# Optimization experiments

Hardware: AMD Instinct MI355X
Metric: run time of the kernel (lower is better)

## Reference

```python
import jax, jax.numpy as jnp
import numpy as np

B, N, C = 4096, 20, 512
S_VIEWS = 8
N_VIEWS = 20


def setup_inputs() -> dict:
    key = jax.random.key(0)
    k1, k2, k3, k4 = jax.random.split(key, 4)
    F0 = jax.random.normal(k1, (B, N, C), dtype=jnp.float32)
    vertices0 = jax.random.normal(k2, (B, N, 3), dtype=jnp.float32)
    W1 = jax.random.normal(k3, (C, 256), dtype=jnp.float32) * 0.04
    b1 = jnp.zeros((256,), dtype=jnp.float32)
    W2 = jax.random.normal(k4, (256, 40), dtype=jnp.float32) * 0.06
    b2 = jnp.zeros((40,), dtype=jnp.float32)
    return {"F0": F0, "vertices0": vertices0, "W1": W1, "b1": b1, "W2": W2, "b2": b2, "k": 8}


def _cls(x, W1, b1, W2, b2):
    # Linear(512,256) -> LeakyReLU(0.2) -> Linear(256,40)
    h = x @ W1 + b1
    h = jnp.where(h > 0, h, 0.2 * h)
    return h @ W2 + b2


def reference(F0, vertices0, W1, b1, W2, b2, k):
    # F0: [B, N, C]; vertices0: [B, N, 3]
    pooled_F = jnp.sum(F0, axis=1) / N_VIEWS                 # [B, C]
    pred = jnp.argmax(_cls(pooled_F, W1, b1, W2, b2), -1)    # [B] predicted class per sample
    score = _cls(F0, W1, b1, W2, b2)                         # [B, N, 40]
    # score[arange(B), :, pred] -> per-view score of the predicted class
    score_F = jnp.take_along_axis(score, pred[:, None, None], axis=2)[..., 0]  # [B, N]
    _, idx = jax.lax.top_k(score_F, S_VIEWS)                 # [B, S]
    F_new = jnp.take_along_axis(F0, idx[:, :, None], axis=1)            # [B, S, C]
    vertices_new = jnp.take_along_axis(vertices0, idx[:, :, None], axis=1)  # [B, S, 3]
    return (F_new, score, vertices_new)
```

## Files before the change

### kernel.cpp

```cpp
#include <hip/hip_runtime.h>
#include <cstdint>

#define BB 4096
#define NV 20
#define CC 512
#define HH 256
#define NC 40
#define SV 8
#define GG 3
#define TAU 2e-4f

typedef short short8 __attribute__((ext_vector_type(8)));
typedef float f32x4 __attribute__((ext_vector_type(4)));
typedef unsigned short ushort4v __attribute__((ext_vector_type(4)));

__device__ __forceinline__ unsigned short f2bf(float x) {
    unsigned u = __float_as_uint(x);
    unsigned r = (u + 0x7FFFu + ((u >> 16) & 1u)) >> 16;
    return (unsigned short)r;
}
__device__ __forceinline__ float bf2f(unsigned short h) {
    return __uint_as_float(((unsigned)h) << 16);
}

#define MFMA16(A, B, C) __builtin_amdgcn_mfma_f32_16x16x32_bf16(A, B, C, 0, 0, 0)
#define BC8(x) __builtin_bit_cast(short8, x)

__global__ void w1pack_kernel(const float* __restrict__ W1,
                              unsigned short* __restrict__ w1fh,
                              unsigned short* __restrict__ w1fl) {
    int e = blockIdx.x * 256 + threadIdx.x;
    int j3 = e & 7, kq = (e >> 3) & 3, n = (e >> 5) & 255, ks = e >> 13;
    int k = ks * 32 + kq * 8 + j3;
    float x = W1[k * HH + n];
    unsigned short h = f2bf(x);
    w1fh[e] = h;
    w1fl[e] = f2bf(x - bf2f(h));
}

__global__ void w2pack_kernel(const float* __restrict__ W2,
                              unsigned short* __restrict__ w2fh,
                              unsigned short* __restrict__ w2fl) {
    int e = blockIdx.x * 256 + threadIdx.x;
    int j3 = e & 7, kq = (e >> 3) & 3;
    int t = e >> 5;
    int n = t % 48, ks = t / 48;
    int k = ks * 32 + kq * 8 + j3;
    float x = (n < NC) ? W2[k * NC + n] : 0.f;
    unsigned short h = f2bf(x);
    w2fh[e] = h;
    w2fl[e] = f2bf(x - bf2f(h));
}

__global__ __launch_bounds__(256, 3) void fused_kernel(
    const float* __restrict__ F0, const float* __restrict__ V0,
    const float* __restrict__ W1, const float* __restrict__ b1,
    const float* __restrict__ W2, const float* __restrict__ b2,
    const unsigned short* __restrict__ w1fh, const unsigned short* __restrict__ w1fl,
    const unsigned short* __restrict__ w2fh, const unsigned short* __restrict__ w2fl,
    int* __restrict__ rflag, int* __restrict__ rpred,
    float* __restrict__ outF, float* __restrict__ outS, float* __restrict__ outV)
{
    const int blk = blockIdx.x;
    const int j = threadIdx.x;
    const int L = j & 63, wq = j >> 6, l15 = L & 15, kq = L >> 4;

    __shared__ __align__(16) char lds[46944];
    __shared__ int idx8[GG][SV];

    unsigned short* Ahi0 = (unsigned short*)lds;
    unsigned short* Alo0 = Ahi0 + 64 * 72;
    unsigned short* Ahi1 = (unsigned short*)(lds + 18432);
    unsigned short* Alo1 = Ahi1 + 64 * 72;
    unsigned short* Hhi  = (unsigned short*)lds;
    unsigned short* Hlo  = Hhi + 32 * 264;
    float*  Sc      = (float*)(lds + 36864);

    f32x4 acc[4][4];
#pragma unroll
    for (int mt = 0; mt < 4; ++mt)
#pragma unroll
        for (int nt = 0; nt < 4; ++nt) acc[mt][nt] = (f32x4){0.f, 0.f, 0.f, 0.f};

    const float4* srcp[4];
    int ldst[4];
    bool sval[4];
#pragma unroll
    for (int i = 0; i < 4; ++i) {
        int f = j + 256 * i;
        int row = f >> 4, k4 = f & 15;
        sval[i] = (row < 60);
        int bi = (row >= 40) ? 2 : (row >= 20) ? 1 : 0;
        int r = row - 20 * bi;
        int batch = blk * GG + bi; if (batch > BB - 1) batch = BB - 1;
        srcp[i] = (const float4*)(F0 + ((size_t)batch * NV + r) * CC) + k4;
        ldst[i] = row * 72 + k4 * 4;
    }

    float4 rv[4];
    auto STAGE_LOAD = [&](int kc) {
#pragma unroll
        for (int i = 0; i < 4; ++i)
            if (sval[i]) rv[i] = srcp[i][kc * 16];
    };
    auto STAGE_CONVERT = [&](unsigned short* __restrict__ Ah,
                             unsigned short* __restrict__ Al) {
#pragma unroll
        for (int i = 0; i < 4; ++i) {
            ushort4v hv = {0, 0, 0, 0}, lv = {0, 0, 0, 0};
            if (sval[i]) {
                float4 x = rv[i];
                hv.x = f2bf(x.x); lv.x = f2bf(x.x - bf2f(hv.x));
                hv.y = f2bf(x.y); lv.y = f2bf(x.y - bf2f(hv.y));
                hv.z = f2bf(x.z); lv.z = f2bf(x.z - bf2f(hv.z));
                hv.w = f2bf(x.w); lv.w = f2bf(x.w - bf2f(hv.w));
            }
            *(ushort4v*)&Ah[ldst[i]] = hv;
            *(ushort4v*)&Al[ldst[i]] = lv;
        }
    };

    const uint4* Bh = (const uint4*)w1fh;
    const uint4* Bl = (const uint4*)w1fl;

    STAGE_LOAD(0);
    STAGE_CONVERT(Ahi0, Alo0);
    STAGE_LOAD(1);
    __syncthreads();

    unsigned short *Ahc = Ahi0, *Alc = Alo0, *Ahn = Ahi1, *Aln = Alo1;
    for (int kc = 0; kc < 8; ++kc) {
        if (kc < 7) {
            STAGE_CONVERT(Ahn, Aln);
            if (kc < 6) STAGE_LOAD(kc + 2);
        }
#pragma unroll
        for (int ks_l = 0; ks_l < 2; ++ks_l) {
            int ks = kc * 2 + ks_l;
            uint4 bh[4], bl[4];
#pragma unroll
            for (int nt = 0; nt < 4; ++nt) {
                int bi1 = (ks * 256 + wq * 64 + nt * 16 + l15) * 4 + kq;
                bh[nt] = Bh[bi1]; bl[nt] = Bl[bi1];
            }
#pragma unroll
            for (int mt = 0; mt < 4; ++mt) {
                int off = (mt * 16 + l15) * 72 + ks_l * 32 + kq * 8;
                short8 Ah = BC8(*(const uint4*)&Ahc[off]);
                short8 Al = BC8(*(const uint4*)&Alc[off]);
#pragma unroll
                for (int nt = 0; nt < 4; ++nt) {
                    short8 Bhv = BC8(bh[nt]), Blv = BC8(bl[nt]);
                    acc[mt][nt] = MFMA16(Ah, Bhv, acc[mt][nt]);
                    acc[mt][nt] = MFMA16(Ah, Blv, acc[mt][nt]);
                    acc[mt][nt] = MFMA16(Al, Bhv, acc[mt][nt]);
                }
            }
        }
        __syncthreads();
        unsigned short* t;
        t = Ahc; Ahc = Ahn; Ahn = t;
        t = Alc; Alc = Aln; Aln = t;
    }

    const uint4* B2h = (const uint4*)w2fh;
    const uint4* B2l = (const uint4*)w2fl;
#pragma unroll
    for (int p = 0; p < 2; ++p) {
        __syncthreads();
#pragma unroll
        for (int mt2 = 0; mt2 < 2; ++mt2) {
            int mt = 2 * p + mt2;
            bool skip = (p == 1 && mt2 == 1 && kq == 3);
#pragma unroll
            for (int nt = 0; nt < 4; ++nt) {
                int col = wq * 64 + nt * 16 + l15;
                float bc = b1[col];
#pragma unroll
                for (int reg = 0; reg < 4; ++reg) {
                    int hb = mt2 * 16 + kq * 4 + reg;
                    float h = acc[mt][nt][reg] + bc;
                    h = (h > 0.f) ? h : 0.2f * h;
                    if (!skip) {
                        unsigned short hh = f2bf(h);
                        Hhi[hb * 264 + col] = hh;
                        Hlo[hb * 264 + col] = f2bf(h - bf2f(hh));
                    }
                }
            }
        }
        if (p == 1) {
#pragma unroll
            for (int nt = 0; nt < 4; ++nt) {
                int col = wq * 64 + nt * 16 + l15;
                float p0 = 0.f, p1 = 0.f, p2 = 0.f;
#pragma unroll
                for (int mt = 0; mt < 4; ++mt)
#pragma unroll
                    for (int reg = 0; reg < 4; ++reg) {
                        int g = mt * 16 + kq * 4 + reg;
                        float v = acc[mt][nt][reg];
                        p0 += (g < 20) ? v : 0.f;
                        p1 += (g >= 20 && g < 40) ? v : 0.f;
                        p2 += (g >= 40 && g < 60) ? v : 0.f;
                    }
                p0 += __shfl_xor(p0, 16); p0 += __shfl_xor(p0, 32);
                p1 += __shfl_xor(p1, 16); p1 += __shfl_xor(p1, 32);
                p2 += __shfl_xor(p2, 16); p2 += __shfl_xor(p2, 32);
                if (kq < 3) {
                    float s = (kq == 0) ? p0 : (kq == 1) ? p1 : p2;
                    float h = s * (1.0f / NV) + b1[col];
                    h = (h > 0.f) ? h : 0.2f * h;
                    unsigned short hh = f2bf(h);
                    Hhi[(28 + kq) * 264 + col] = hh;
                    Hlo[(28 + kq) * 264 + col] = f2bf(h - bf2f(hh));
                } else {
                    Hhi[31 * 264 + col] = 0;
                    Hlo[31 * 264 + col] = 0;
                }
            }
        }
        __syncthreads();

        if (wq < 3) {
            f32x4 sacc[2];
            sacc[0] = (f32x4){0.f, 0.f, 0.f, 0.f};
            sacc[1] = (f32x4){0.f, 0.f, 0.f, 0.f};
            for (int ks2 = 0; ks2 < 8; ++ks2) {
                int bi2 = (ks2 * 48 + wq * 16 + l15) * 4 + kq;
                short8 Bhv = BC8(B2h[bi2]), Blv = BC8(B2l[bi2]);
#pragma unroll
                for (int tt = 0; tt < 2; ++tt) {
                    int off = (tt * 16 + l15) * 264 + ks2 * 32 + kq * 8;
                    short8 Ah2 = BC8(*(const uint4*)&Hhi[off]);
                    short8 Al2 = BC8(*(const uint4*)&Hlo[off]);
                    sacc[tt] = MFMA16(Ah2, Bhv, sacc[tt]);
                    sacc[tt] = MFMA16(Ah2, Blv, sacc[tt]);
                    sacc[tt] = MFMA16(Al2, Bhv, sacc[tt]);
                }
            }
            int cls = wq * 16 + l15;
            if (cls < NC) {
                float bc2 = b2[cls];
#pragma unroll
                for (int tt = 0; tt < 2; ++tt)
#pragma unroll
                    for (int reg = 0; reg < 4; ++reg) {
                        int lm = 32 * p + tt * 16 + kq * 4 + reg;
                        float sv = sacc[tt][reg] + bc2;
                        if (lm < 60) {
                            int bi = (lm >= 40) ? 2 : (lm >= 20) ? 1 : 0;
                            int r = lm - 20 * bi;
                            Sc[bi * 840 + r * NC + cls] = sv;
                        } else if (lm < 63) {
                            Sc[(lm - 60) * 840 + NV * NC + cls] = sv;
                        }
                    }
            }
        }
    }
    __syncthreads();

    if (j < GG) {
        const float* sp = &Sc[j * 840 + NV * NC];
        int p = 0;
        float m1 = sp[0];
        for (int c = 1; c < NC; ++c)
            if (sp[c] > m1) { m1 = sp[c]; p = c; }
        float m2 = -1e30f;
        for (int c = 0; c < NC; ++c)
            if (c != p && sp[c] > m2) m2 = sp[c];
        int f0 = (m1 - m2 < TAU) ? 1 : 0;

        float v[NV];
#pragma unroll
        for (int n = 0; n < NV; ++n) v[n] = Sc[j * 840 + n * NC + p];
        int ord[9];
        float vals[9];
        unsigned taken = 0;
#pragma unroll
        for (int s = 0; s < 9; ++s) {
            int bi = 0;
            float bv = -1e30f;
#pragma unroll
            for (int n = 0; n < NV; ++n)
                if (!((taken >> n) & 1u) && v[n] > bv) { bv = v[n]; bi = n; }
            taken |= 1u << bi;
            ord[s] = bi;
            vals[s] = bv;
        }
        int fix = 0;
#pragma unroll
        for (int s = 0; s < 8; ++s)
            if (vals[s] - vals[s + 1] < TAU) fix = 1;
#pragma unroll
        for (int s = 0; s < SV; ++s) idx8[j][s] = ord[s];

        int batch = blk * GG + j; if (batch > BB - 1) batch = BB - 1;
        rflag[batch] = f0 ? 1 : (fix ? 2 : 0);
        rpred[batch] = p;
    }
    __syncthreads();

    for (int t = j; t < GG * NV * NC; t += 256) {
        int bi = t / 800, o = t - bi * 800;
        int batch = blk * GG + bi; if (batch > BB - 1) batch = BB - 1;
        outS[(size_t)batch * (NV * NC) + o] = Sc[bi * 840 + o];
    }

    for (int t = j; t < GG * SV * (CC / 4); t += 256) {
        int bi = t >> 10;
        int s = (t >> 7) & 7;
        int t4 = t & 127;
        int batch = blk * GG + bi; if (batch > BB - 1) batch = BB - 1;
        int row = idx8[bi][s];
        const float4* src = (const float4*)(F0 + ((size_t)batch * NV + row) * CC);
        float4* dst = (float4*)(outF + ((size_t)batch * SV + s) * CC);
        dst[t4] = src[t4];
    }

    if (j < GG * SV * 3) {
        int bi = j / 24, o = j - bi * 24;
        int s = o / 3, d = o - s * 3;
        int batch = blk * GG + bi; if (batch > BB - 1) batch = BB - 1;
        outV[((size_t)batch * SV + s) * 3 + d] =
            V0[((size_t)batch * NV + idx8[bi][s]) * 3 + d];
    }
}

__global__ __launch_bounds__(256) void rescue_kernel(
    const float* __restrict__ F0, const float* __restrict__ V0,
    const float* __restrict__ W1, const float* __restrict__ b1,
    const float* __restrict__ W2, const float* __restrict__ b2,
    const int* __restrict__ rflag, const int* __restrict__ rpred,
    float* __restrict__ outF, float* __restrict__ outV)
{
    const int b = blockIdx.x;
    const int flag = rflag[b];
    if (flag == 0) return;

    const int j = threadIdx.x;
    const int L = j & 63, wq = j >> 6;

    __shared__ __align__(16) float Xf[NV * CC];
    __shared__ double pooledD[CC];
    __shared__ double Dbuf[HH];
    __shared__ double Sd[NC];
    __shared__ double part[NV][4];
    __shared__ double SFdS[NV];
    __shared__ int predSh;
    __shared__ int idxs[SV];

    const float* Xb = F0 + (size_t)b * (NV * CC);
    for (int t = j; t < NV * CC / 4; t += 256)
        ((float4*)Xf)[t] = ((const float4*)Xb)[t];
    __syncthreads();

    if (flag == 1) {
        for (int c = j; c < CC; c += 256) {
            double s = 0.0;
            for (int r = 0; r < NV; ++r) s += (double)Xf[r * CC + c];
            pooledD[c] = s / (double)NV;
        }
        __syncthreads();
        double a = 0.0;
        for (int c = 0; c < CC; ++c) a += pooledD[c] * (double)W1[c * HH + j];
        double h = a + (double)b1[j];
        h = (h > 0.0) ? h : 0.2 * h;
        Dbuf[j] = h;
        __syncthreads();
        if (j < NC) {
            double s = 0.0;
            for (int k = 0; k < HH; ++k) s += Dbuf[k] * (double)W2[k * NC + j];
            Sd[j] = s + (double)b2[j];
        }
        __syncthreads();
        if (j == 0) {
            int p = 0;
            double m = Sd[0];
            for (int c = 1; c < NC; ++c)
                if (Sd[c] > m) { m = Sd[c]; p = c; }
            predSh = p;
        }
        __syncthreads();
    } else {
        if (j == 0) predSh = rpred[b];
        __syncthreads();
    }
    const int p = predSh;

    const double b1d = (double)b1[j];
    const double w2jp = (double)W2[j * NC + p];
#pragma unroll
    for (int half = 0; half < 2; ++half) {
        double a[10];
#pragma unroll
        for (int r = 0; r < 10; ++r) a[r] = 0.0;
        for (int c = 0; c < CC; c += 4) {
            double w0 = (double)W1[(c + 0) * HH + j];
            double w1v = (double)W1[(c + 1) * HH + j];
            double w2v = (double)W1[(c + 2) * HH + j];
            double w3v = (double)W1[(c + 3) * HH + j];
#pragma unroll
            for (int r = 0; r < 10; ++r) {
                const float4 x = *(const float4*)&Xf[(half * 10 + r) * CC + c];
                a[r] += (double)x.x * w0;
                a[r] += (double)x.y * w1v;
                a[r] += (double)x.z * w2v;
                a[r] += (double)x.w * w3v;
            }
        }
#pragma unroll
        for (int r = 0; r < 10; ++r) {
            double h = a[r] + b1d;
            h = (h > 0.0) ? h : 0.2 * h;
            double val = h * w2jp;
#pragma unroll
            for (int off = 32; off >= 1; off >>= 1)
                val += __shfl_xor(val, off);
            if (L == 0) part[half * 10 + r][wq] = val;
        }
    }
    __syncthreads();
    if (j < NV)
        SFdS[j] = part[j][0] + part[j][1] + part[j][2] + part[j][3]
                + (double)b2[p];
    __syncthreads();
    if (j == 0) {
        unsigned taken = 0;
        for (int s = 0; s < SV; ++s) {
            int bsel = 0;
            double bv = -1e300;
            for (int n = 0; n < NV; ++n)
                if (!((taken >> n) & 1u) && SFdS[n] > bv) { bv = SFdS[n]; bsel = n; }
            taken |= 1u << bsel;
            idxs[s] = bsel;
        }
    }
    __syncthreads();

    for (int t = j; t < SV * (CC / 4); t += 256) {
        int s = t >> 7, t4 = t & 127;
        int row = idxs[s];
        ((float4*)(outF + ((size_t)b * SV + s) * CC))[t4] =
            ((const float4*)(F0 + ((size_t)b * NV + row) * CC))[t4];
    }
    if (j < SV * 3) {
        int s = j / 3, d = j - s * 3;
        outV[((size_t)b * SV + s) * 3 + d] =
            V0[((size_t)b * NV + idxs[s]) * 3 + d];
    }
}

extern "C" void kernel_launch(void* const* d_in, const int* in_sizes, int n_in,
                              void* d_out, int out_size, void* d_ws, size_t ws_size,
                              hipStream_t stream) {
    const float* F0 = (const float*)d_in[0];
    const float* V0 = (const float*)d_in[1];
    const float* W1 = (const float*)d_in[2];
    const float* b1 = (const float*)d_in[3];
    const float* W2 = (const float*)d_in[4];
    const float* b2 = (const float*)d_in[5];

    char* ws = (char*)d_ws;
    unsigned short* w1fh = (unsigned short*)ws;
    unsigned short* w1fl = (unsigned short*)(ws + 262144);
    unsigned short* w2fh = (unsigned short*)(ws + 524288);
    unsigned short* w2fl = (unsigned short*)(ws + 548864);
    int* rflag = (int*)(ws + 573440);
    int* rpred = (int*)(ws + 589824);

    float* out = (float*)d_out;
    float* outF = out;
    float* outS = out + (size_t)BB * SV * CC;
    float* outV = outS + (size_t)BB * NV * NC;

    w1pack_kernel<<<512, 256, 0, stream>>>(W1, w1fh, w1fl);
    w2pack_kernel<<<48, 256, 0, stream>>>(W2, w2fh, w2fl);
    fused_kernel<<<(BB + GG - 1) / GG, 256, 0, stream>>>(
        F0, V0, W1, b1, W2, b2, w1fh, w1fl, w2fh, w2fl, rflag, rpred,
        outF, outS, outV);
    rescue_kernel<<<BB, 256, 0, stream>>>(
        F0, V0, W1, b1, W2, b2, rflag, rpred, outF, outV);
}
```

Measured before the change: 464.8 us.

## Compact rescue work into atomic worklist, fuse pack kernels, write scores directly

Merges the two weight-pack kernels into one launch that also resets a worklist counter. The fused kernel now writes per-view scores straight to global memory instead of staging them in LDS, which shrinks shared memory and raises the occupancy hint from 3 to 4 blocks. Flagged batches are appended to a compact worklist with an atomic, so the rescue kernel launches 256 persistent blocks that loop over it rather than 4096 mostly-empty blocks. The top-k selection now reads scores back from global memory, and the rescue kernel keeps 20 double accumulators per thread, which may raise register pressure.

Measured after the change: 693.6 us. +49.2%, slower.

```diff
diff --git a/kernel.cpp b/kernel.cpp
--- a/kernel.cpp
+++ b/kernel.cpp
@@ -26,46 +26,48 @@
 #define MFMA16(A, B, C) __builtin_amdgcn_mfma_f32_16x16x32_bf16(A, B, C, 0, 0, 0)
 #define BC8(x) __builtin_bit_cast(short8, x)
 
-__global__ void w1pack_kernel(const float* __restrict__ W1,
-                              unsigned short* __restrict__ w1fh,
-                              unsigned short* __restrict__ w1fl) {
+__global__ void pack_kernel(const float* __restrict__ W1,
+                            const float* __restrict__ W2,
+                            unsigned short* __restrict__ w1fh,
+                            unsigned short* __restrict__ w1fl,
+                            unsigned short* __restrict__ w2fh,
+                            unsigned short* __restrict__ w2fl,
+                            int* __restrict__ wcount) {
     int e = blockIdx.x * 256 + threadIdx.x;
-    int j3 = e & 7, kq = (e >> 3) & 3, n = (e >> 5) & 255, ks = e >> 13;
-    int k = ks * 32 + kq * 8 + j3;
-    float x = W1[k * HH + n];
-    unsigned short h = f2bf(x);
-    w1fh[e] = h;
-    w1fl[e] = f2bf(x - bf2f(h));
-}
-
-__global__ void w2pack_kernel(const float* __restrict__ W2,
-                              unsigned short* __restrict__ w2fh,
-                              unsigned short* __restrict__ w2fl) {
-    int e = blockIdx.x * 256 + threadIdx.x;
-    int j3 = e & 7, kq = (e >> 3) & 3;
-    int t = e >> 5;
-    int n = t % 48, ks = t / 48;
-    int k = ks * 32 + kq * 8 + j3;
-    float x = (n < NC) ? W2[k * NC + n] : 0.f;
-    unsigned short h = f2bf(x);
-    w2fh[e] = h;
-    w2fl[e] = f2bf(x - bf2f(h));
-}
-
-__global__ __launch_bounds__(256, 3) void fused_kernel(
+    if (e == 0) *wcount = 0;
+    {
+        int j3 = e & 7, kq = (e >> 3) & 3, n = (e >> 5) & 255, ks = e >> 13;
+        int k = ks * 32 + kq * 8 + j3;
+        float x = W1[k * HH + n];
+        unsigned short h = f2bf(x);
+        w1fh[e] = h;
+        w1fl[e] = f2bf(x - bf2f(h));
+    }
+    if (e < 12288) {
+        int j3 = e & 7, kq = (e >> 3) & 3;
+        int t = e >> 5;
+        int n = t % 48, ks = t / 48;
+        int k = ks * 32 + kq * 8 + j3;
+        float x = (n < NC) ? W2[k * NC + n] : 0.f;
+        unsigned short h = f2bf(x);
+        w2fh[e] = h;
+        w2fl[e] = f2bf(x - bf2f(h));
+    }
+}
+
+__global__ __launch_bounds__(256, 4) void fused_kernel(
     const float* __restrict__ F0, const float* __restrict__ V0,
-    const float* __restrict__ W1, const float* __restrict__ b1,
-    const float* __restrict__ W2, const float* __restrict__ b2,
+    const float* __restrict__ b1, const float* __restrict__ b2,
     const unsigned short* __restrict__ w1fh, const unsigned short* __restrict__ w1fl,
     const unsigned short* __restrict__ w2fh, const unsigned short* __restrict__ w2fl,
-    int* __restrict__ rflag, int* __restrict__ rpred,
+    int* __restrict__ wcount, int* __restrict__ wl, int* __restrict__ rpred,
     float* __restrict__ outF, float* __restrict__ outS, float* __restrict__ outV)
 {
     const int blk = blockIdx.x;
     const int j = threadIdx.x;
     const int L = j & 63, wq = j >> 6, l15 = L & 15, kq = L >> 4;
 
-    __shared__ __align__(16) char lds[46944];
+    __shared__ __align__(16) char lds[37376];
     __shared__ int idx8[GG][SV];
 
     unsigned short* Ahi0 = (unsigned short*)lds;
@@ -74,7 +76,7 @@
     unsigned short* Alo1 = Ahi1 + 64 * 72;
     unsigned short* Hhi  = (unsigned short*)lds;
     unsigned short* Hlo  = Hhi + 32 * 264;
-    float*  Sc      = (float*)(lds + 36864);
+    float* ScP = (float*)(lds + 36864);
 
     f32x4 acc[4][4];
 #pragma unroll
@@ -251,9 +253,10 @@
                         if (lm < 60) {
                             int bi = (lm >= 40) ? 2 : (lm >= 20) ? 1 : 0;
                             int r = lm - 20 * bi;
-                            Sc[bi * 840 + r * NC + cls] = sv;
+                            int batch = blk * GG + bi; if (batch > BB - 1) batch = BB - 1;
+                            outS[(size_t)batch * (NV * NC) + r * NC + cls] = sv;
                         } else if (lm < 63) {
-                            Sc[(lm - 60) * 840 + NV * NC + cls] = sv;
+                            ScP[(lm - 60) * NC + cls] = sv;
                         }
                     }
             }
@@ -262,7 +265,8 @@
     __syncthreads();
 
     if (j < GG) {
-        const float* sp = &Sc[j * 840 + NV * NC];
+        int batch = blk * GG + j; if (batch > BB - 1) batch = BB - 1;
+        const float* sp = &ScP[j * NC];
         int p = 0;
         float m1 = sp[0];
         for (int c = 1; c < NC; ++c)
@@ -272,9 +276,10 @@
             if (c != p && sp[c] > m2) m2 = sp[c];
         int f0 = (m1 - m2 < TAU) ? 1 : 0;
 
+        const float* so = outS + (size_t)batch * (NV * NC);
         float v[NV];
 #pragma unroll
-        for (int n = 0; n < NV; ++n) v[n] = Sc[j * 840 + n * NC + p];
+        for (int n = 0; n < NV; ++n) v[n] = so[n * NC + p];
         int ord[9];
         float vals[9];
         unsigned taken = 0;
@@ -296,17 +301,17 @@
 #pragma unroll
         for (int s = 0; s < SV; ++s) idx8[j][s] = ord[s];
 
-        int batch = blk * GG + j; if (batch > BB - 1) batch = BB - 1;
-        rflag[batch] = f0 ? 1 : (fix ? 2 : 0);
-        rpred[batch] = p;
+        int batch0 = blk * GG + j;
+        if (batch0 < BB) {
+            rpred[batch0] = p;
+            int flagv = f0 ? 1 : (fix ? 2 : 0);
+            if (flagv) {
+                int slot = atomicAdd(wcount, 1);
+                wl[slot] = batch0 * 4 + flagv;
+            }
+        }
     }
     __syncthreads();
-
-    for (int t = j; t < GG * NV * NC; t += 256) {
-        int bi = t / 800, o = t - bi * 800;
-        int batch = blk * GG + bi; if (batch > BB - 1) batch = BB - 1;
-        outS[(size_t)batch * (NV * NC) + o] = Sc[bi * 840 + o];
-    }
 
     for (int t = j; t < GG * SV * (CC / 4); t += 256) {
         int bi = t >> 10;
@@ -332,12 +337,12 @@
     const float* __restrict__ F0, const float* __restrict__ V0,
     const float* __restrict__ W1, const float* __restrict__ b1,
     const float* __restrict__ W2, const float* __restrict__ b2,
-    const int* __restrict__ rflag, const int* __restrict__ rpred,
+    const int* __restrict__ wcount, const int* __restrict__ wl,
+    const int* __restrict__ rpred,
     float* __restrict__ outF, float* __restrict__ outV)
 {
-    const int b = blockIdx.x;
-    const int flag = rflag[b];
-    if (flag == 0) return;
+    const int cnt = *wcount;
+    if ((int)blockIdx.x >= cnt) return;
 
     const int j = threadIdx.x;
     const int L = j & 63, wq = j >> 6;
@@ -351,59 +356,62 @@
     __shared__ int predSh;
     __shared__ int idxs[SV];
 
-    const float* Xb = F0 + (size_t)b * (NV * CC);
-    for (int t = j; t < NV * CC / 4; t += 256)
-        ((float4*)Xf)[t] = ((const float4*)Xb)[t];
-    __syncthreads();
-
-    if (flag == 1) {
-        for (int c = j; c < CC; c += 256) {
-            double s = 0.0;
-            for (int r = 0; r < NV; ++r) s += (double)Xf[r * CC + c];
-            pooledD[c] = s / (double)NV;
-        }
-        __syncthreads();
-        double a = 0.0;
-        for (int c = 0; c < CC; ++c) a += pooledD[c] * (double)W1[c * HH + j];
-        double h = a + (double)b1[j];
-        h = (h > 0.0) ? h : 0.2 * h;
-        Dbuf[j] = h;
-        __syncthreads();
-        if (j < NC) {
-            double s = 0.0;
-            for (int k = 0; k < HH; ++k) s += Dbuf[k] * (double)W2[k * NC + j];
-            Sd[j] = s + (double)b2[j];
-        }
-        __syncthreads();
-        if (j == 0) {
-            int p = 0;
-            double m = Sd[0];
-            for (int c = 1; c < NC; ++c)
-                if (Sd[c] > m) { m = Sd[c]; p = c; }
-            predSh = p;
-        }
-        __syncthreads();
-    } else {
-        if (j == 0) predSh = rpred[b];
-        __syncthreads();
-    }
-    const int p = predSh;
-
-    const double b1d = (double)b1[j];
-    const double w2jp = (double)W2[j * NC + p];
-#pragma unroll
-    for (int half = 0; half < 2; ++half) {
-        double a[10];
-#pragma unroll
-        for (int r = 0; r < 10; ++r) a[r] = 0.0;
+    for (int w = blockIdx.x; w < cnt; w += 256) {
+        const int e = wl[w];
+        const int b = e >> 2;
+        const int flag = e & 3;
+
+        const float* Xb = F0 + (size_t)b * (NV * CC);
+        for (int t = j; t < NV * CC / 4; t += 256)
+            ((float4*)Xf)[t] = ((const float4*)Xb)[t];
+        __syncthreads();
+
+        if (flag == 1) {
+            for (int c = j; c < CC; c += 256) {
+                double s = 0.0;
+                for (int r = 0; r < NV; ++r) s += (double)Xf[r * CC + c];
+                pooledD[c] = s / (double)NV;
+            }
+            __syncthreads();
+            double a = 0.0;
+            for (int c = 0; c < CC; ++c) a += pooledD[c] * (double)W1[c * HH + j];
+            double h = a + (double)b1[j];
+            h = (h > 0.0) ? h : 0.2 * h;
+            Dbuf[j] = h;
+            __syncthreads();
+            if (j < NC) {
+                double s = 0.0;
+                for (int k = 0; k < HH; ++k) s += Dbuf[k] * (double)W2[k * NC + j];
+                Sd[j] = s + (double)b2[j];
+            }
+            __syncthreads();
+            if (j == 0) {
+                int p = 0;
+                double m = Sd[0];
+                for (int c = 1; c < NC; ++c)
+                    if (Sd[c] > m) { m = Sd[c]; p = c; }
+                predSh = p;
+            }
+            __syncthreads();
+        } else {
+            if (j == 0) predSh = rpred[b];
+            __syncthreads();
+        }
+        const int p = predSh;
+
+        const double b1d = (double)b1[j];
+        const double w2jp = (double)W2[j * NC + p];
+        double a[NV];
+#pragma unroll
+        for (int r = 0; r < NV; ++r) a[r] = 0.0;
         for (int c = 0; c < CC; c += 4) {
             double w0 = (double)W1[(c + 0) * HH + j];
             double w1v = (double)W1[(c + 1) * HH + j];
             double w2v = (double)W1[(c + 2) * HH + j];
             double w3v = (double)W1[(c + 3) * HH + j];
 #pragma unroll
-            for (int r = 0; r < 10; ++r) {
-                const float4 x = *(const float4*)&Xf[(half * 10 + r) * CC + c];
+            for (int r = 0; r < NV; ++r) {
+                const float4 x = *(const float4*)&Xf[r * CC + c];
                 a[r] += (double)x.x * w0;
                 a[r] += (double)x.y * w1v;
                 a[r] += (double)x.z * w2v;
@@ -411,44 +419,45 @@
             }
         }
 #pragma unroll
-        for (int r = 0; r < 10; ++r) {
+        for (int r = 0; r < NV; ++r) {
             double h = a[r] + b1d;
             h = (h > 0.0) ? h : 0.2 * h;
             double val = h * w2jp;
 #pragma unroll
             for (int off = 32; off >= 1; off >>= 1)
                 val += __shfl_xor(val, off);
-            if (L == 0) part[half * 10 + r][wq] = val;
-        }
-    }
-    __syncthreads();
-    if (j < NV)
-        SFdS[j] = part[j][0] + part[j][1] + part[j][2] + part[j][3]
-                + (double)b2[p];
-    __syncthreads();
-    if (j == 0) {
-        unsigned taken = 0;
-        for (int s = 0; s < SV; ++s) {
-            int bsel = 0;
-            double bv = -1e300;
-            for (int n = 0; n < NV; ++n)
-                if (!((taken >> n) & 1u) && SFdS[n] > bv) { bv = SFdS[n]; bsel = n; }
-            taken |= 1u << bsel;
-            idxs[s] = bsel;
-        }
-    }
-    __syncthreads();
-
-    for (int t = j; t < SV * (CC / 4); t += 256) {
-        int s = t >> 7, t4 = t & 127;
-        int row = idxs[s];
-        ((float4*)(outF + ((size_t)b * SV + s) * CC))[t4] =
-            ((const float4*)(F0 + ((size_t)b * NV + row) * CC))[t4];
-    }
-    if (j < SV * 3) {
-        int s = j / 3, d = j - s * 3;
-        outV[((size_t)b * SV + s) * 3 + d] =
-            V0[((size_t)b * NV + idxs[s]) * 3 + d];
+            if (L == 0) part[r][wq] = val;
+        }
+        __syncthreads();
+        if (j < NV)
+            SFdS[j] = part[j][0] + part[j][1] + part[j][2] + part[j][3]
+                    + (double)b2[p];
+        __syncthreads();
+        if (j == 0) {
+            unsigned taken = 0;
+            for (int s = 0; s < SV; ++s) {
+                int bsel = 0;
+                double bv = -1e300;
+                for (int n = 0; n < NV; ++n)
+                    if (!((taken >> n) & 1u) && SFdS[n] > bv) { bv = SFdS[n]; bsel = n; }
+                taken |= 1u << bsel;
+                idxs[s] = bsel;
+            }
+        }
+        __syncthreads();
+
+        for (int t = j; t < SV * (CC / 4); t += 256) {
+            int s = t >> 7, t4 = t & 127;
+            int row = idxs[s];
+            ((float4*)(outF + ((size_t)b * SV + s) * CC))[t4] =
+                ((const float4*)(F0 + ((size_t)b * NV + row) * CC))[t4];
+        }
+        if (j < SV * 3) {
+            int s = j / 3, d = j - s * 3;
+            outV[((size_t)b * SV + s) * 3 + d] =
+                V0[((size_t)b * NV + idxs[s]) * 3 + d];
+        }
+        __syncthreads();
     }
 }
 
@@ -467,19 +476,19 @@
     unsigned short* w1fl = (unsigned short*)(ws + 262144);
     unsigned short* w2fh = (unsigned short*)(ws + 524288);
     unsigned short* w2fl = (unsigned short*)(ws + 548864);
-    int* rflag = (int*)(ws + 573440);
-    int* rpred = (int*)(ws + 589824);
+    int* wcount = (int*)(ws + 573440);
+    int* wl     = (int*)(ws + 573504);
+    int* rpred  = (int*)(ws + 589888);
 
     float* out = (float*)d_out;
     float* outF = out;
     float* outS = out + (size_t)BB * SV * CC;
     float* outV = outS + (size_t)BB * NV * NC;
 
-    w1pack_kernel<<<512, 256, 0, stream>>>(W1, w1fh, w1fl);
-    w2pack_kernel<<<48, 256, 0, stream>>>(W2, w2fh, w2fl);
+    pack_kernel<<<512, 256, 0, stream>>>(W1, W2, w1fh, w1fl, w2fh, w2fl, wcount);
     fused_kernel<<<(BB + GG - 1) / GG, 256, 0, stream>>>(
-        F0, V0, W1, b1, W2, b2, w1fh, w1fl, w2fh, w2fl, rflag, rpred,
+        F0, V0, b1, b2, w1fh, w1fl, w2fh, w2fl, wcount, wl, rpred,
         outF, outS, outV);
-    rescue_kernel<<<BB, 256, 0, stream>>>(
-        F0, V0, W1, b1, W2, b2, rflag, rpred, outF, outV);
-}
+    rescue_kernel<<<256, 256, 0, stream>>>(
+        F0, V0, W1, b1, W2, b2, wcount, wl, rpred, outF, outV);
+}
```
